# Kernel tuning notes

Measured on AMD Instinct MI355X. Metric: run time of the kernel, lower is better.

## Reference

```python
import jax, jax.numpy as jnp
import numpy as np

NBIT = 8
NSPLIT = 255.0  # 2**NBIT - 1


def _quantized_matmul(x, w_clean, eps):
    # Faithful port of quantization(): bit-slice x into NBIT binary planes, run a
    # noisy linear per plane with weight w + randn*|w|*0.1, and sum. The 8
    # sequential fc() calls are fused into one einsum over the bit axis.
    # x: (..., in); w_clean: (out, in); eps: (NBIT, out, in) standard normal.
    mn = jnp.min(x)
    mx = jnp.max(x)
    q = ((x - mn) / (mx - mn) * NSPLIT).astype(jnp.uint8).astype(jnp.int32)  # truncating cast as in torch
    quant_base = 2 ** jnp.arange(NBIT, dtype=jnp.int32)
    binary = ((q[..., None] & quant_base) != 0).astype(x.dtype)              # (..., in, NBIT)
    scaled = binary * (2.0 ** jnp.arange(NBIT)).astype(x.dtype)              # plane i scaled by 2**i
    w_noisy = w_clean[None] + eps * jnp.abs(w_clean)[None] * 0.1             # (NBIT, out, in)
    z = jnp.einsum('...ib,boi->...o', scaled, w_noisy)
    return z, mn, mx, w_noisy[-1]  # fc.weight after loop == last noisy weight


def _forward(node_embedding, edge_embedding, nbr_mask, cond1, cond2, eps1, eps2, bn_gamma, bn_beta):
    B, At, Nbr, Fe = edge_embedding.shape
    Fn = node_embedding.shape[-1]
    c1 = jnp.concatenate(
        [jnp.broadcast_to(node_embedding[:, :, None, :], (B, At, Nbr, Fn)), edge_embedding],
        axis=3)                                                              # (B, At, Nbr, Fn+Fe)
    # quantization + re_quantization through fc (re-quant uses last noisy fc.weight)
    z1, mn1, mx1, w_last = _quantized_matmul(c1, cond1[0], eps1)
    bias1 = jnp.sum(mn1 * w_last, axis=1)                                    # (H1,)
    h = jax.nn.relu(z1 / NSPLIT * (mx1 - mn1) + bias1)                       # (B, At, Nbr, H1)
    # quantization + re_quantization through fc_2 (re-quant uses conductance[1][-1])
    z2, mn2, mx2, _ = _quantized_matmul(h, cond2[0], eps2)
    bias2 = jnp.sum(mn2 * cond2[-1], axis=1)                                 # (2*Fn,)
    c2 = z2 / NSPLIT * (mx2 - mn2) + bias2                                   # (B, At, Nbr, 2*Fn)
    nbr_gate, nbr_extract = jnp.split(c2, 2, axis=3)
    nbr_sumed = jax.nn.sigmoid(nbr_gate) * jnp.tanh(nbr_extract) * nbr_mask[..., None]
    nbr_sumed = jnp.sum(nbr_sumed, axis=2)                                   # (B, At, Fn)
    # BatchNorm1d in training mode: batch statistics over flattened (B*At)
    flat = nbr_sumed.reshape(-1, Fn)
    mean = jnp.mean(flat, axis=0)
    var = jnp.var(flat, axis=0)  # biased variance, as torch BN uses for normalization
    bn = ((flat - mean) / jnp.sqrt(var + 1e-5) * bn_gamma + bn_beta).reshape(B, At, Fn)
    return jax.nn.relu(node_embedding + bn)


def setup_inputs() -> dict:
    key = jax.random.key(0)
    ks = jax.random.split(key, 7)
    B, At, Nbr, Fn, Fe = 16, 96, 12, 64, 64
    H1, H2 = 4 * (Fn + Fe), 2 * Fn
    return {
        'node_embedding': jax.random.normal(ks[0], (B, At, Fn), jnp.float32),
        'edge_embedding': jax.random.normal(ks[1], (B, At, Nbr, Fe), jnp.float32),
        'nbr_mask': (jax.random.uniform(ks[2], (B, At, Nbr)) > 0.5).astype(jnp.float32),
        'cond1': jax.random.normal(ks[3], (2, H1, Fn + Fe), jnp.float32) * 0.05,
        'cond2': jax.random.normal(ks[4], (2, H2, H1), jnp.float32) * 0.05,
        'eps1': jax.random.normal(ks[5], (NBIT, H1, Fn + Fe), jnp.float32),
        'eps2': jax.random.normal(ks[6], (NBIT, H2, H1), jnp.float32),
        'bn_gamma': jnp.ones((Fn,), jnp.float32),
        'bn_beta': jnp.zeros((Fn,), jnp.float32),
    }


def reference(node_embedding, edge_embedding, nbr_mask, cond1, cond2, eps1, eps2, bn_gamma, bn_beta):
    return _forward(node_embedding, edge_embedding, nbr_mask, cond1, cond2, eps1, eps2, bn_gamma, bn_beta)
```

## Files before the change

### kernel.cpp

```cpp
#include <hip/hip_runtime.h>
#include <stdint.h>

#define B_    16
#define AT_   96
#define NBR_  12
#define FN_   64
#define FE_   64
#define M1    (B_*AT_*NBR_)
#define R_    (B_*AT_)
#define K1Q   128
#define N1    512
#define K2Q   512
#define N2    128
#define SPLIT2 4

typedef _Float16 f16x8 __attribute__((ext_vector_type(8)));
typedef float    f32x4 __attribute__((ext_vector_type(4)));
typedef __attribute__((address_space(1))) const void gconst_void;
typedef __attribute__((address_space(3))) void lds_void;

#define OFF_SCAL  0u
#define OFF_B1R   256u
#define OFF_B2R   (OFF_B1R + 2048u)
#define OFF_Q1    4096u
#define OFF_W1E   (OFF_Q1  + (size_t)M1*K1Q)
#define OFF_W2E   (OFF_W1E + (size_t)N1*K1Q*8*2)
#define OFF_Q2    (OFF_W2E + (size_t)N2*K2Q*8*2)
#define OFF_H     (OFF_Q2  + (size_t)M1*K2Q)
#define OFF_ZP    OFF_H
#define OFF_NS    (OFF_H   + (size_t)M1*N1*4)

__device__ __forceinline__ unsigned int enc_f(float f) {
    unsigned int u = __float_as_uint(f);
    return (u & 0x80000000u) ? ~u : (u | 0x80000000u);
}
__device__ __forceinline__ float dec_f(unsigned int u) {
    return __uint_as_float((u & 0x80000000u) ? (u & 0x7FFFFFFFu) : ~u);
}

__global__ void k_init(unsigned int* scal, float* b1raw, float* b2raw) {
    int t = threadIdx.x;
    if (t == 0) { scal[0] = 0xFFFFFFFFu; scal[1] = 0u; scal[2] = 0xFFFFFFFFu; scal[3] = 0u; }
    if (t < N1) b1raw[t] = 0.f;
    if (t < N2) b2raw[t] = 0.f;
}

__global__ __launch_bounds__(256) void k_minmax_c1(const float* __restrict__ node,
                                                   const float* __restrict__ edge,
                                                   unsigned int* __restrict__ scal) {
    const int nn = B_*AT_*FN_;
    const int ntot = nn + M1*FE_;
    float mn = 3.0e38f, mx = -3.0e38f;
    for (int idx = blockIdx.x*blockDim.x + threadIdx.x; idx < ntot; idx += gridDim.x*blockDim.x) {
        float x = (idx < nn) ? node[idx] : edge[idx - nn];
        mn = fminf(mn, x); mx = fmaxf(mx, x);
    }
    __shared__ float smn[256], smx[256];
    smn[threadIdx.x] = mn; smx[threadIdx.x] = mx; __syncthreads();
    for (int s = 128; s > 0; s >>= 1) {
        if (threadIdx.x < s) {
            smn[threadIdx.x] = fminf(smn[threadIdx.x], smn[threadIdx.x+s]);
            smx[threadIdx.x] = fmaxf(smx[threadIdx.x], smx[threadIdx.x+s]);
        }
        __syncthreads();
    }
    if (threadIdx.x == 0) { atomicMin(&scal[0], enc_f(smn[0])); atomicMax(&scal[1], enc_f(smx[0])); }
}

template<int KQ, int N, int SBASE, bool USE_SECOND>
__global__ __launch_bounds__(256) void k_prep_w16(const float* __restrict__ w_clean,
                                                  const float* __restrict__ eps,
                                                  const unsigned int* __restrict__ scal,
                                                  float* __restrict__ braw,
                                                  _Float16* __restrict__ We) {
    int idx = blockIdx.x*blockDim.x + threadIdx.x;
    if (idx >= N*KQ) return;
    int o = idx / KQ;
    int i = idx % KQ;
    float mn = dec_f(scal[SBASE]), mx = dec_f(scal[SBASE+1]);
    float s = (mx - mn) * (1.0f/255.0f);
    float w = w_clean[idx];
    float aw = fabsf(w) * 0.1f;
    union { _Float16 h[8]; uint4 u; } pk;
    float p = s;
    float v7 = 0.f;
    #pragma unroll
    for (int b = 0; b < 8; b++) {
        float e = eps[(size_t)b*N*KQ + idx];
        float v = w + e*aw;
        if (b == 7) v7 = v;
        pk.h[b] = (_Float16)(v * p);
        p *= 2.0f;
    }
    *(uint4*)&We[((size_t)o*KQ + i)*8] = pk.u;
    float bv = USE_SECOND ? w_clean[(size_t)N*KQ + idx] : v7;
    #pragma unroll
    for (int off = 32; off > 0; off >>= 1) bv += __shfl_down(bv, off);
    if ((threadIdx.x & 63) == 0) atomicAdd(&braw[o], bv);
}

__global__ __launch_bounds__(256) void k_quant_c1(const float* __restrict__ node,
                                                  const float* __restrict__ edge,
                                                  const unsigned int* __restrict__ scal,
                                                  unsigned int* __restrict__ q1) {
    int idx = blockIdx.x*256 + threadIdx.x;
    int m = idx >> 5, dw = idx & 31;
    const float mn = dec_f(scal[0]), rng = dec_f(scal[1]) - mn;
    float4 x;
    if (dw < 16) x = *(const float4*)&node[(m/NBR_)*FN_ + dw*4];
    else         x = *(const float4*)&edge[(size_t)m*FE_ + (dw-16)*4];
    unsigned int b0 = (unsigned char)(int)((x.x - mn) / rng * 255.0f);
    unsigned int b1 = (unsigned char)(int)((x.y - mn) / rng * 255.0f);
    unsigned int b2 = (unsigned char)(int)((x.z - mn) / rng * 255.0f);
    unsigned int b3 = (unsigned char)(int)((x.w - mn) / rng * 255.0f);
    q1[idx] = b0 | (b1 << 8) | (b2 << 16) | (b3 << 24);
}

__global__ __launch_bounds__(256) void k_quant_h(const float* __restrict__ h,
                                                 const unsigned int* __restrict__ scal,
                                                 unsigned int* __restrict__ q2) {
    int idx = blockIdx.x*256 + threadIdx.x;
    const float mn = dec_f(scal[2]), rng = dec_f(scal[3]) - mn;
    float4 x = *(const float4*)&h[(size_t)idx*4];
    unsigned int b0 = (unsigned char)(int)((x.x - mn) / rng * 255.0f);
    unsigned int b1 = (unsigned char)(int)((x.y - mn) / rng * 255.0f);
    unsigned int b2 = (unsigned char)(int)((x.z - mn) / rng * 255.0f);
    unsigned int b3 = (unsigned char)(int)((x.w - mn) / rng * 255.0f);
    q2[idx] = b0 | (b1 << 8) | (b2 << 16) | (b3 << 24);
}

__device__ __forceinline__ f16x8 expand_byte(unsigned int byte) {
    unsigned int r2 = byte | (byte << 15);
    union { unsigned int u[4]; f16x8 h; } t;
    t.u[0] = ( r2       & 0x00010001u) * 0x3C00u;
    t.u[1] = ((r2 >> 2) & 0x00010001u) * 0x3C00u;
    t.u[2] = ((r2 >> 4) & 0x00010001u) * 0x3C00u;
    t.u[3] = ((r2 >> 6) & 0x00010001u) * 0x3C00u;
    return t.h;
}

template<int KQ, int N, int SPLITK, bool EPI1>
__global__ __launch_bounds__(256, 4) void kg(const unsigned char* __restrict__ q,
                                             const _Float16* __restrict__ W,
                                             const float* __restrict__ braw,
                                             void* __restrict__ outv,
                                             unsigned int* __restrict__ scal) {
    constexpr int KP  = KQ * 8;
    constexpr int KPS = KP / SPLITK;
    __shared__ _Float16 Bs[8192];
    __shared__ uint2    Qs[256];

    const int tid  = threadIdx.x;
    const int lane = tid & 63;
    const int w    = tid >> 6;
    const int wm   = (w & 1) * 64;
    const int kg   = w >> 1;
    const int l15  = lane & 15;
    const int lq   = lane >> 4;
    const int sh8  = lq * 8;
    const int m0   = blockIdx.x * 128;
    const int o0   = blockIdx.y * 64;
    const int kbase = blockIdx.z * KPS;

    f32x4 acc[4][4] = {};

    const int akg = tid >> 7, agt = tid & 127;
    const unsigned char* aq = q + (size_t)(m0 + agt)*KQ + (kbase >> 3) + akg*64;

    #pragma unroll 1
    for (int it = 0; it < KPS/128; ++it) {
        __syncthreads();
        uint2 qa = *(const uint2*)(aq + it*8);
        #pragma unroll
        for (int iss = 0; iss < 4; ++iss) {
            int s    = iss*256 + tid;
            int skg  = s >> 9;
            int sg   = s & 511;
            int n    = sg >> 3;
            int csrc = (sg & 7) ^ (n & 7);
            const _Float16* gp = W + (size_t)(o0 + n)*KP + kbase + skg*512 + it*64 + csrc*8;
            _Float16* lp = &Bs[(size_t)(iss*256 + (tid & ~63)) * 8];
            __builtin_amdgcn_global_load_lds((gconst_void*)gp, (lds_void*)lp, 16, 0, 0);
        }
        Qs[(akg << 7) + agt] = qa;
        __builtin_amdgcn_s_waitcnt(0);
        __syncthreads();

        uint2 qd[4];
        #pragma unroll
        for (int mf = 0; mf < 4; ++mf)
            qd[mf] = Qs[kg*128 + wm + mf*16 + l15];
        #pragma unroll
        for (int kf = 0; kf < 2; ++kf) {
            f16x8 bf[4];
            #pragma unroll
            for (int nf = 0; nf < 4; ++nf) {
                const int nl = nf*16 + l15;
                const int ch = kf*4 + lq;
                bf[nf] = *(const f16x8*)&Bs[kg*4096 + nl*64 + ((ch ^ (nl & 7)) << 3)];
            }
            #pragma unroll
            for (int mf = 0; mf < 4; ++mf) {
                unsigned int byte = ((kf ? qd[mf].y : qd[mf].x) >> sh8) & 0xFFu;
                f16x8 a = expand_byte(byte);
                #pragma unroll
                for (int nf = 0; nf < 4; ++nf)
                    acc[mf][nf] = __builtin_amdgcn_mfma_f32_16x16x32_f16(a, bf[nf], acc[mf][nf], 0, 0, 0);
            }
        }
    }

    float* red = (float*)Bs;
    #pragma unroll
    for (int nf = 0; nf < 4; ++nf) {
        __syncthreads();
        if (kg == 1) {
            #pragma unroll
            for (int mf = 0; mf < 4; ++mf)
                *(f32x4*)&red[(w & 1)*1024 + mf*256 + lane*4] = acc[mf][nf];
        }
        __syncthreads();
        if (kg == 0) {
            #pragma unroll
            for (int mf = 0; mf < 4; ++mf)
                acc[mf][nf] += *(const f32x4*)&red[(w & 1)*1024 + mf*256 + lane*4];
        }
    }

    if (EPI1) {
        float tmn = 3.0e38f, tmx = -3.0e38f;
        if (kg == 0) {
            float* out = (float*)outv;
            const float mn1 = dec_f(scal[0]);
            float bv[4];
            #pragma unroll
            for (int nf = 0; nf < 4; ++nf) bv[nf] = mn1 * braw[o0 + nf*16 + l15];
            #pragma unroll
            for (int mf = 0; mf < 4; ++mf) {
                const int mr = m0 + wm + mf*16 + lq*4;
                #pragma unroll
                for (int nf = 0; nf < 4; ++nf) {
                    const int oc = o0 + nf*16 + l15;
                    #pragma unroll
                    for (int r = 0; r < 4; ++r) {
                        float v = acc[mf][nf][r] + bv[nf];
                        v = fmaxf(v, 0.0f);
                        tmn = fminf(tmn, v); tmx = fmaxf(tmx, v);
                        out[(size_t)(mr + r)*N + oc] = v;
                    }
                }
            }
        }
        __syncthreads();
        red[tid] = tmn; red[256 + tid] = tmx;
        __syncthreads();
        for (int s = 128; s > 0; s >>= 1) {
            if (tid < s) {
                red[tid]       = fminf(red[tid],       red[tid + s]);
                red[256 + tid] = fmaxf(red[256 + tid], red[256 + tid + s]);
            }
            __syncthreads();
        }
        if (tid == 0) { atomicMin(&scal[2], enc_f(red[0])); atomicMax(&scal[3], enc_f(red[256])); }
    } else {
        if (kg == 0) {
            _Float16* op = (_Float16*)outv + (size_t)blockIdx.z * ((size_t)M1 * N);
            #pragma unroll
            for (int mf = 0; mf < 4; ++mf) {
                const int mr = m0 + wm + mf*16 + lq*4;
                #pragma unroll
                for (int nf = 0; nf < 4; ++nf) {
                    const int oc = o0 + nf*16 + l15;
                    #pragma unroll
                    for (int r = 0; r < 4; ++r)
                        op[(size_t)(mr + r)*N + oc] = (_Float16)acc[mf][nf][r];
                }
            }
        }
    }
}

__global__ __launch_bounds__(256) void k_nbr(const _Float16* __restrict__ zp,
                                             const float* __restrict__ b2raw,
                                             const unsigned int* __restrict__ scal,
                                             const float* __restrict__ mask,
                                             float* __restrict__ ns) {
    const size_t SP = (size_t)M1 * N2;
    int tid = threadIdx.x;
    int r = blockIdx.x*4 + (tid >> 6);
    int f = tid & 63;
    const float mn2 = dec_f(scal[2]);
    float bg = mn2 * b2raw[f], be = mn2 * b2raw[64 + f];
    float s = 0.f;
    #pragma unroll
    for (int n = 0; n < NBR_; n++) {
        int m = r*NBR_ + n;
        size_t base = (size_t)m * N2;
        float g = bg, e = be;
        #pragma unroll
        for (int z = 0; z < SPLIT2; z++) {
            g += (float)zp[z*SP + base + f];
            e += (float)zp[z*SP + base + 64 + f];
        }
        float sig = 1.0f / (1.0f + expf(-g));
        s += sig * tanhf(e) * mask[m];
    }
    ns[r*64 + f] = s;
}

__global__ __launch_bounds__(256) void k_bn(const float* __restrict__ ns,
                                            const float* __restrict__ node,
                                            const float* __restrict__ gamma,
                                            const float* __restrict__ beta,
                                            float* __restrict__ out) {
    int f = blockIdx.x;
    int tid = threadIdx.x;
    float x[6];
    float s = 0.f, ss = 0.f;
    #pragma unroll
    for (int k = 0; k < 6; k++) {
        int r = tid + k*256;
        x[k] = ns[r*64 + f];
        s += x[k]; ss += x[k]*x[k];
    }
    __shared__ float rs[256], rss[256];
    rs[tid] = s; rss[tid] = ss; __syncthreads();
    for (int st = 128; st > 0; st >>= 1) {
        if (tid < st) { rs[tid] += rs[tid+st]; rss[tid] += rss[tid+st]; }
        __syncthreads();
    }
    float mean = rs[0] / 1536.0f;
    float var  = rss[0] / 1536.0f - mean*mean;
    float denom = sqrtf(var + 1e-5f);
    float g = gamma[f], bt = beta[f];
    #pragma unroll
    for (int k = 0; k < 6; k++) {
        int r = tid + k*256;
        float v = node[r*64 + f] + ((x[k] - mean) / denom * g + bt);
        out[r*64 + f] = fmaxf(v, 0.f);
    }
}

extern "C" void kernel_launch(void* const* d_in, const int* in_sizes, int n_in,
                              void* d_out, int out_size, void* d_ws, size_t ws_size,
                              hipStream_t stream) {
    const float* node  = (const float*)d_in[0];
    const float* edge  = (const float*)d_in[1];
    const float* mask  = (const float*)d_in[2];
    const float* cond1 = (const float*)d_in[3];
    const float* cond2 = (const float*)d_in[4];
    const float* eps1  = (const float*)d_in[5];
    const float* eps2  = (const float*)d_in[6];
    const float* gamma = (const float*)d_in[7];
    const float* beta  = (const float*)d_in[8];
    float* out = (float*)d_out;
    char* ws = (char*)d_ws;

    unsigned int*  scal = (unsigned int*)(ws + OFF_SCAL);
    float* b1raw = (float*)(ws + OFF_B1R);
    float* b2raw = (float*)(ws + OFF_B2R);
    unsigned char* q1 = (unsigned char*)(ws + OFF_Q1);
    _Float16* W1e = (_Float16*)(ws + OFF_W1E);
    _Float16* W2e = (_Float16*)(ws + OFF_W2E);
    unsigned char* q2 = (unsigned char*)(ws + OFF_Q2);
    float*    h  = (float*)(ws + OFF_H);
    _Float16* zp = (_Float16*)(ws + OFF_ZP);
    float*    ns = (float*)(ws + OFF_NS);

    k_init<<<1, 1024, 0, stream>>>(scal, b1raw, b2raw);
    k_minmax_c1<<<512, 256, 0, stream>>>(node, edge, scal);
    k_prep_w16<K1Q, N1, 0, false><<<(N1*K1Q + 255)/256, 256, 0, stream>>>(cond1, eps1, scal, b1raw, W1e);
    k_quant_c1<<<(M1*32)/256, 256, 0, stream>>>(node, edge, scal, (unsigned int*)q1);
    kg<K1Q, N1, 1, true><<<dim3(M1/128, N1/64, 1), 256, 0, stream>>>(q1, W1e, b1raw, h, scal);
    k_prep_w16<K2Q, N2, 2, true><<<(N2*K2Q + 255)/256, 256, 0, stream>>>(cond2, eps2, scal, b2raw, W2e);
    k_quant_h<<<(M1*128)/256, 256, 0, stream>>>(h, scal, (unsigned int*)q2);
    kg<K2Q, N2, SPLIT2, false><<<dim3(M1/128, N2/64, SPLIT2), 256, 0, stream>>>(q2, W2e, b2raw, zp, scal);
    k_nbr<<<R_/4, 256, 0, stream>>>(zp, b2raw, scal, mask, ns);
    k_bn<<<64, 256, 0, stream>>>(ns, node, gamma, beta, out);
}
```

Baseline: 198.8 us.

## Drop LDS staging in bit-plane GEMM, store hidden as fp16, vectorize loads

The GEMM kernel no longer stages weights and quantized activations through LDS with async global-to-LDS loads and no longer splits K across waves. Each wave now loads its A bytes and B fp16 fragments straight from global memory into registers, covering 64 rows, so the K-split reduction through shared memory is gone. The intermediate hidden activation is stored as fp16 instead of fp32, which halves its write and re-read traffic, and min/max is taken on the rounded values. The min/max, quantize and neighbour kernels also get wider vector loads. The trade-offs are that weights are re-read from global or cache by every wave with no reuse through LDS, and the fp16 hidden may change quantization bins slightly.

After: 264.2 us. +32.9%, slower.

```diff
diff --git a/kernel.cpp b/kernel.cpp
--- a/kernel.cpp
+++ b/kernel.cpp
@@ -15,9 +15,8 @@
 #define SPLIT2 4
 
 typedef _Float16 f16x8 __attribute__((ext_vector_type(8)));
+typedef _Float16 f16x2 __attribute__((ext_vector_type(2)));
 typedef float    f32x4 __attribute__((ext_vector_type(4)));
-typedef __attribute__((address_space(1))) const void gconst_void;
-typedef __attribute__((address_space(3))) void lds_void;
 
 #define OFF_SCAL  0u
 #define OFF_B1R   256u
@@ -28,7 +27,7 @@
 #define OFF_Q2    (OFF_W2E + (size_t)N2*K2Q*8*2)
 #define OFF_H     (OFF_Q2  + (size_t)M1*K2Q)
 #define OFF_ZP    OFF_H
-#define OFF_NS    (OFF_H   + (size_t)M1*N1*4)
+#define OFF_NS    (OFF_H   + (size_t)M1*N1*2)
 
 __device__ __forceinline__ unsigned int enc_f(float f) {
     unsigned int u = __float_as_uint(f);
@@ -48,12 +47,13 @@
 __global__ __launch_bounds__(256) void k_minmax_c1(const float* __restrict__ node,
                                                    const float* __restrict__ edge,
                                                    unsigned int* __restrict__ scal) {
-    const int nn = B_*AT_*FN_;
-    const int ntot = nn + M1*FE_;
+    const int nn4 = (B_*AT_*FN_)/4;
+    const int tot4 = nn4 + (M1*FE_)/4;
     float mn = 3.0e38f, mx = -3.0e38f;
-    for (int idx = blockIdx.x*blockDim.x + threadIdx.x; idx < ntot; idx += gridDim.x*blockDim.x) {
-        float x = (idx < nn) ? node[idx] : edge[idx - nn];
-        mn = fminf(mn, x); mx = fmaxf(mx, x);
+    for (int idx = blockIdx.x*blockDim.x + threadIdx.x; idx < tot4; idx += gridDim.x*blockDim.x) {
+        float4 x = (idx < nn4) ? ((const float4*)node)[idx] : ((const float4*)edge)[idx - nn4];
+        mn = fminf(mn, fminf(fminf(x.x, x.y), fminf(x.z, x.w)));
+        mx = fmaxf(mx, fmaxf(fmaxf(x.x, x.y), fmaxf(x.z, x.w)));
     }
     __shared__ float smn[256], smx[256];
     smn[threadIdx.x] = mn; smx[threadIdx.x] = mx; __syncthreads();
@@ -116,17 +116,25 @@
     q1[idx] = b0 | (b1 << 8) | (b2 << 16) | (b3 << 24);
 }
 
-__global__ __launch_bounds__(256) void k_quant_h(const float* __restrict__ h,
+__global__ __launch_bounds__(256) void k_quant_h(const _Float16* __restrict__ h,
                                                  const unsigned int* __restrict__ scal,
                                                  unsigned int* __restrict__ q2) {
     int idx = blockIdx.x*256 + threadIdx.x;
     const float mn = dec_f(scal[2]), rng = dec_f(scal[3]) - mn;
-    float4 x = *(const float4*)&h[(size_t)idx*4];
-    unsigned int b0 = (unsigned char)(int)((x.x - mn) / rng * 255.0f);
-    unsigned int b1 = (unsigned char)(int)((x.y - mn) / rng * 255.0f);
-    unsigned int b2 = (unsigned char)(int)((x.z - mn) / rng * 255.0f);
-    unsigned int b3 = (unsigned char)(int)((x.w - mn) / rng * 255.0f);
-    q2[idx] = b0 | (b1 << 8) | (b2 << 16) | (b3 << 24);
+    f16x8 v = *(const f16x8*)(h + (size_t)idx*8);
+    unsigned int lo = 0, hi = 0;
+    #pragma unroll
+    for (int j = 0; j < 4; j++) {
+        float x = (float)v[j];
+        lo |= ((unsigned int)(unsigned char)(int)((x - mn) / rng * 255.0f)) << (j*8);
+    }
+    #pragma unroll
+    for (int j = 0; j < 4; j++) {
+        float x = (float)v[4+j];
+        hi |= ((unsigned int)(unsigned char)(int)((x - mn) / rng * 255.0f)) << (j*8);
+    }
+    uint2 o; o.x = lo; o.y = hi;
+    *(uint2*)&q2[idx*2] = o;
 }
 
 __device__ __forceinline__ f16x8 expand_byte(unsigned int byte) {
@@ -140,118 +148,83 @@
 }
 
 template<int KQ, int N, int SPLITK, bool EPI1>
-__global__ __launch_bounds__(256, 4) void kg(const unsigned char* __restrict__ q,
-                                             const _Float16* __restrict__ W,
-                                             const float* __restrict__ braw,
-                                             void* __restrict__ outv,
-                                             unsigned int* __restrict__ scal) {
+__global__ __launch_bounds__(256, 3) void kgd(const unsigned char* __restrict__ q,
+                                              const _Float16* __restrict__ W,
+                                              const float* __restrict__ braw,
+                                              void* __restrict__ outv,
+                                              unsigned int* __restrict__ scal) {
     constexpr int KP  = KQ * 8;
     constexpr int KPS = KP / SPLITK;
-    __shared__ _Float16 Bs[8192];
-    __shared__ uint2    Qs[256];
-
     const int tid  = threadIdx.x;
     const int lane = tid & 63;
     const int w    = tid >> 6;
-    const int wm   = (w & 1) * 64;
-    const int kg   = w >> 1;
     const int l15  = lane & 15;
     const int lq   = lane >> 4;
     const int sh8  = lq * 8;
-    const int m0   = blockIdx.x * 128;
+    const int m0   = blockIdx.x * 256 + w * 64;
     const int o0   = blockIdx.y * 64;
     const int kbase = blockIdx.z * KPS;
 
     f32x4 acc[4][4] = {};
 
-    const int akg = tid >> 7, agt = tid & 127;
-    const unsigned char* aq = q + (size_t)(m0 + agt)*KQ + (kbase >> 3) + akg*64;
+    unsigned int aoff[4];
+    #pragma unroll
+    for (int mf = 0; mf < 4; ++mf)
+        aoff[mf] = (unsigned int)(m0 + mf*16 + l15) * KQ + (kbase >> 3);
+    unsigned int boff[8];
+    #pragma unroll
+    for (int nf = 0; nf < 4; ++nf)
+        #pragma unroll
+        for (int kf = 0; kf < 2; ++kf)
+            boff[nf*2+kf] = (unsigned int)(o0 + nf*16 + l15) * KP + kbase + kf*32 + lq*8;
 
     #pragma unroll 1
-    for (int it = 0; it < KPS/128; ++it) {
-        __syncthreads();
-        uint2 qa = *(const uint2*)(aq + it*8);
-        #pragma unroll
-        for (int iss = 0; iss < 4; ++iss) {
-            int s    = iss*256 + tid;
-            int skg  = s >> 9;
-            int sg   = s & 511;
-            int n    = sg >> 3;
-            int csrc = (sg & 7) ^ (n & 7);
-            const _Float16* gp = W + (size_t)(o0 + n)*KP + kbase + skg*512 + it*64 + csrc*8;
-            _Float16* lp = &Bs[(size_t)(iss*256 + (tid & ~63)) * 8];
-            __builtin_amdgcn_global_load_lds((gconst_void*)gp, (lds_void*)lp, 16, 0, 0);
-        }
-        Qs[(akg << 7) + agt] = qa;
-        __builtin_amdgcn_s_waitcnt(0);
-        __syncthreads();
-
+    for (int it = 0; it < KPS/64; ++it) {
         uint2 qd[4];
         #pragma unroll
         for (int mf = 0; mf < 4; ++mf)
-            qd[mf] = Qs[kg*128 + wm + mf*16 + l15];
+            qd[mf] = *(const uint2*)(q + aoff[mf] + it*8);
+        f16x8 bf[8];
+        #pragma unroll
+        for (int j = 0; j < 8; ++j)
+            bf[j] = *(const f16x8*)(W + boff[j] + it*64);
         #pragma unroll
         for (int kf = 0; kf < 2; ++kf) {
-            f16x8 bf[4];
-            #pragma unroll
-            for (int nf = 0; nf < 4; ++nf) {
-                const int nl = nf*16 + l15;
-                const int ch = kf*4 + lq;
-                bf[nf] = *(const f16x8*)&Bs[kg*4096 + nl*64 + ((ch ^ (nl & 7)) << 3)];
-            }
             #pragma unroll
             for (int mf = 0; mf < 4; ++mf) {
                 unsigned int byte = ((kf ? qd[mf].y : qd[mf].x) >> sh8) & 0xFFu;
                 f16x8 a = expand_byte(byte);
                 #pragma unroll
                 for (int nf = 0; nf < 4; ++nf)
-                    acc[mf][nf] = __builtin_amdgcn_mfma_f32_16x16x32_f16(a, bf[nf], acc[mf][nf], 0, 0, 0);
+                    acc[mf][nf] = __builtin_amdgcn_mfma_f32_16x16x32_f16(a, bf[nf*2+kf], acc[mf][nf], 0, 0, 0);
             }
         }
     }
 
-    float* red = (float*)Bs;
-    #pragma unroll
-    for (int nf = 0; nf < 4; ++nf) {
-        __syncthreads();
-        if (kg == 1) {
+    if (EPI1) {
+        __shared__ float red[512];
+        _Float16* out = (_Float16*)outv;
+        const float mn1 = dec_f(scal[0]);
+        float bv[4];
+        #pragma unroll
+        for (int nf = 0; nf < 4; ++nf) bv[nf] = mn1 * braw[o0 + nf*16 + l15];
+        float tmn = 3.0e38f, tmx = -3.0e38f;
+        #pragma unroll
+        for (int mf = 0; mf < 4; ++mf) {
+            const int mr = m0 + mf*16 + lq*4;
             #pragma unroll
-            for (int mf = 0; mf < 4; ++mf)
-                *(f32x4*)&red[(w & 1)*1024 + mf*256 + lane*4] = acc[mf][nf];
-        }
-        __syncthreads();
-        if (kg == 0) {
-            #pragma unroll
-            for (int mf = 0; mf < 4; ++mf)
-                acc[mf][nf] += *(const f32x4*)&red[(w & 1)*1024 + mf*256 + lane*4];
-        }
-    }
-
-    if (EPI1) {
-        float tmn = 3.0e38f, tmx = -3.0e38f;
-        if (kg == 0) {
-            float* out = (float*)outv;
-            const float mn1 = dec_f(scal[0]);
-            float bv[4];
-            #pragma unroll
-            for (int nf = 0; nf < 4; ++nf) bv[nf] = mn1 * braw[o0 + nf*16 + l15];
-            #pragma unroll
-            for (int mf = 0; mf < 4; ++mf) {
-                const int mr = m0 + wm + mf*16 + lq*4;
+            for (int nf = 0; nf < 4; ++nf) {
+                const int oc = o0 + nf*16 + l15;
                 #pragma unroll
-                for (int nf = 0; nf < 4; ++nf) {
-                    const int oc = o0 + nf*16 + l15;
-                    #pragma unroll
-                    for (int r = 0; r < 4; ++r) {
-                        float v = acc[mf][nf][r] + bv[nf];
-                        v = fmaxf(v, 0.0f);
-                        tmn = fminf(tmn, v); tmx = fmaxf(tmx, v);
-                        out[(size_t)(mr + r)*N + oc] = v;
-                    }
+                for (int r = 0; r < 4; ++r) {
+                    float v = fmaxf(acc[mf][nf][r] + bv[nf], 0.0f);
+                    _Float16 v16 = (_Float16)v;
+                    float vr = (float)v16;
+                    tmn = fminf(tmn, vr); tmx = fmaxf(tmx, vr);
+                    out[(size_t)(mr + r)*N + oc] = v16;
                 }
             }
         }
-        __syncthreads();
         red[tid] = tmn; red[256 + tid] = tmx;
         __syncthreads();
         for (int s = 128; s > 0; s >>= 1) {
@@ -263,18 +236,16 @@
         }
         if (tid == 0) { atomicMin(&scal[2], enc_f(red[0])); atomicMax(&scal[3], enc_f(red[256])); }
     } else {
-        if (kg == 0) {
-            _Float16* op = (_Float16*)outv + (size_t)blockIdx.z * ((size_t)M1 * N);
+        _Float16* op = (_Float16*)outv + (size_t)blockIdx.z * ((size_t)M1 * N);
+        #pragma unroll
+        for (int mf = 0; mf < 4; ++mf) {
+            const int mr = m0 + mf*16 + lq*4;
             #pragma unroll
-            for (int mf = 0; mf < 4; ++mf) {
-                const int mr = m0 + wm + mf*16 + lq*4;
+            for (int nf = 0; nf < 4; ++nf) {
+                const int oc = o0 + nf*16 + l15;
                 #pragma unroll
-                for (int nf = 0; nf < 4; ++nf) {
-                    const int oc = o0 + nf*16 + l15;
-                    #pragma unroll
-                    for (int r = 0; r < 4; ++r)
-                        op[(size_t)(mr + r)*N + oc] = (_Float16)acc[mf][nf][r];
-                }
+                for (int r = 0; r < 4; ++r)
+                    op[(size_t)(mr + r)*N + oc] = (_Float16)acc[mf][nf][r];
             }
         }
     }
@@ -287,25 +258,30 @@
                                              float* __restrict__ ns) {
     const size_t SP = (size_t)M1 * N2;
     int tid = threadIdx.x;
-    int r = blockIdx.x*4 + (tid >> 6);
-    int f = tid & 63;
+    int r = blockIdx.x*8 + (tid >> 5);
+    int f2 = (tid & 31) * 2;
     const float mn2 = dec_f(scal[2]);
-    float bg = mn2 * b2raw[f], be = mn2 * b2raw[64 + f];
-    float s = 0.f;
+    float bg0 = mn2 * b2raw[f2],      bg1 = mn2 * b2raw[f2+1];
+    float be0 = mn2 * b2raw[64 + f2], be1 = mn2 * b2raw[65 + f2];
+    float s0 = 0.f, s1 = 0.f;
     #pragma unroll
     for (int n = 0; n < NBR_; n++) {
         int m = r*NBR_ + n;
         size_t base = (size_t)m * N2;
-        float g = bg, e = be;
+        float g0 = bg0, g1 = bg1, e0 = be0, e1 = be1;
         #pragma unroll
         for (int z = 0; z < SPLIT2; z++) {
-            g += (float)zp[z*SP + base + f];
-            e += (float)zp[z*SP + base + 64 + f];
-        }
-        float sig = 1.0f / (1.0f + expf(-g));
-        s += sig * tanhf(e) * mask[m];
-    }
-    ns[r*64 + f] = s;
+            f16x2 gv = *(const f16x2*)(zp + z*SP + base + f2);
+            f16x2 ev = *(const f16x2*)(zp + z*SP + base + 64 + f2);
+            g0 += (float)gv[0]; g1 += (float)gv[1];
+            e0 += (float)ev[0]; e1 += (float)ev[1];
+        }
+        float mk = mask[m];
+        s0 += (1.0f / (1.0f + expf(-g0))) * tanhf(e0) * mk;
+        s1 += (1.0f / (1.0f + expf(-g1))) * tanhf(e1) * mk;
+    }
+    float2 o; o.x = s0; o.y = s1;
+    *(float2*)&ns[r*64 + f2] = o;
 }
 
 __global__ __launch_bounds__(256) void k_bn(const float* __restrict__ ns,
@@ -363,7 +339,7 @@
     _Float16* W1e = (_Float16*)(ws + OFF_W1E);
     _Float16* W2e = (_Float16*)(ws + OFF_W2E);
     unsigned char* q2 = (unsigned char*)(ws + OFF_Q2);
-    float*    h  = (float*)(ws + OFF_H);
+    _Float16* h  = (_Float16*)(ws + OFF_H);
     _Float16* zp = (_Float16*)(ws + OFF_ZP);
     float*    ns = (float*)(ws + OFF_NS);
 
@@ -371,10 +347,10 @@
     k_minmax_c1<<<512, 256, 0, stream>>>(node, edge, scal);
     k_prep_w16<K1Q, N1, 0, false><<<(N1*K1Q + 255)/256, 256, 0, stream>>>(cond1, eps1, scal, b1raw, W1e);
     k_quant_c1<<<(M1*32)/256, 256, 0, stream>>>(node, edge, scal, (unsigned int*)q1);
-    kg<K1Q, N1, 1, true><<<dim3(M1/128, N1/64, 1), 256, 0, stream>>>(q1, W1e, b1raw, h, scal);
+    kgd<K1Q, N1, 1, true><<<dim3(M1/256, N1/64, 1), 256, 0, stream>>>(q1, W1e, b1raw, h, scal);
     k_prep_w16<K2Q, N2, 2, true><<<(N2*K2Q + 255)/256, 256, 0, stream>>>(cond2, eps2, scal, b2raw, W2e);
-    k_quant_h<<<(M1*128)/256, 256, 0, stream>>>(h, scal, (unsigned int*)q2);
-    kg<K2Q, N2, SPLIT2, false><<<dim3(M1/128, N2/64, SPLIT2), 256, 0, stream>>>(q2, W2e, b2raw, zp, scal);
-    k_nbr<<<R_/4, 256, 0, stream>>>(zp, b2raw, scal, mask, ns);
+    k_quant_h<<<(M1*512/8)/256, 256, 0, stream>>>(h, scal, (unsigned int*)q2);
+    kgd<K2Q, N2, SPLIT2, false><<<dim3(M1/256, N2/64, SPLIT2), 256, 0, stream>>>(q2, W2e, b2raw, zp, scal);
+    k_nbr<<<R_/8, 256, 0, stream>>>(zp, b2raw, scal, mask, ns);
     k_bn<<<64, 256, 0, stream>>>(ns, node, gamma, beta, out);
 }
```
